# Kernel optimization log

Hardware: AMD Instinct MI355X
Metric: run time of the kernel (lower is better)

## Reference

```python
import jax, jax.numpy as jnp
import numpy as np

B, S, D, F, E, K = 2, 2048, 1024, 1024, 8, 2


def setup_inputs() -> dict:
    key = jax.random.key(0)
    kx, kg, k1, k3, k2 = jax.random.split(key, 5)
    # kaiming_uniform_(a=sqrt(5)) => Uniform(-1/sqrt(fan_in), 1/sqrt(fan_in))
    x = jax.random.normal(kx, (B, S, D), dtype=jnp.float32)
    gate_w = jax.random.uniform(kg, (E, D), jnp.float32, -1.0, 1.0) / np.sqrt(D)
    w1 = jax.random.uniform(k1, (E, F, D), jnp.float32, -1.0, 1.0) / np.sqrt(D)
    w3 = jax.random.uniform(k3, (E, F, D), jnp.float32, -1.0, 1.0) / np.sqrt(D)
    w2 = jax.random.uniform(k2, (E, D, F), jnp.float32, -1.0, 1.0) / np.sqrt(F)
    return {"x": x, "gate_w": gate_w, "w1": w1, "w3": w3, "w2": w2}


def reference(x, gate_w, w1, w3, w2):
    b, s, d = x.shape
    T = b * s
    xf = x.reshape(T, d)                      # [T, D]
    # ---- Gate: softmax scores, top-k selection, renormalized weights ----
    logits = xf @ gate_w.T                    # [T, E]
    probs = jax.nn.softmax(logits, axis=-1)
    topk_w, topk_idx = jax.lax.top_k(probs, K)            # [T, K]
    topk_w = topk_w / jnp.sum(topk_w, axis=-1, keepdims=True)
    # Dense per-token gate matrix [T, E]; zero for unselected experts, so the
    # weighted combine below is exactly sum_k w_k * expert_{idx_k}(x).
    gate_full = jnp.zeros((T, E), x.dtype).at[
        jnp.arange(T)[:, None], topk_idx].add(topk_w)
    # ---- Grouped SwiGLU experts: loop over small fixed E, vectorized over tokens ----
    out = jnp.zeros_like(xf)
    for e in range(E):
        h = jax.nn.silu(xf @ w1[e].T) * (xf @ w3[e].T)    # [T, F]
        out = out + gate_full[:, e:e + 1] * (h @ w2[e].T)  # [T, D]
    return out.reshape(b, s, d)
```

## Files before the change

kernel.cpp:

```cpp
#include <hip/hip_runtime.h>
#include <hip/hip_bf16.h>
#include <cstdint>
#include <cstddef>

#define T_TOK 4096
#define DDIM  1024
#define FDIM  1024
#define NEXP  8

typedef __attribute__((ext_vector_type(8))) short bf16x8;
typedef __attribute__((ext_vector_type(4))) float f32x4;
typedef __attribute__((ext_vector_type(8))) unsigned short u16x8;

__device__ __forceinline__ unsigned short f2bf(float f) {
  unsigned int u = __float_as_uint(f);
  u += 0x7FFFu + ((u >> 16) & 1u);
  return (unsigned short)(u >> 16);
}
__device__ __forceinline__ float bf2f(unsigned short u) {
  return __uint_as_float(((unsigned int)u) << 16);
}

__device__ __forceinline__ void gload_lds16(const void* g, void* l) {
  __builtin_amdgcn_global_load_lds(
      (const __attribute__((address_space(1))) unsigned int*)g,
      (__attribute__((address_space(3))) unsigned int*)l, 16, 0, 0);
}

__device__ __forceinline__ void vwait6() { asm volatile("s_waitcnt vmcnt(6)" ::: "memory"); }
__device__ __forceinline__ void vwait0() { asm volatile("s_waitcnt vmcnt(0)" ::: "memory"); }
__device__ __forceinline__ void lwait0() { asm volatile("s_waitcnt lgkmcnt(0)" ::: "memory"); }
__device__ __forceinline__ void barr()   { asm volatile("s_barrier" ::: "memory"); }

__device__ __forceinline__ bf16x8 frag_ld(const unsigned short* tile, int row, int kk) {
  int byteoff = (row << 7) + ((kk * 2) ^ ((row & 7) << 4));
  return *reinterpret_cast<const bf16x8*>(reinterpret_cast<const char*>(tile) + byteoff);
}

__global__ __launch_bounds__(256) void prep_kernel(
    const float* __restrict__ w1, const float* __restrict__ w3, const float* __restrict__ w2,
    unsigned short* __restrict__ W1b, unsigned short* __restrict__ W3b,
    unsigned short* __restrict__ W2b,
    const float* __restrict__ x, const float* __restrict__ gw,
    unsigned int* __restrict__ Xb32, int* __restrict__ tkidx, float* __restrict__ tkw,
    int* __restrict__ curp) {
  __shared__ float gws[NEXP * DDIM];
  const int bid = blockIdx.x;
  const int tid = threadIdx.x;

  if (bid < 3072) {
    const int sub = bid >> 10;
    const int b = bid & 1023;
    const float* s = (sub == 0) ? w1 : (sub == 1) ? w3 : w2;
    unsigned short* d = (sub == 0) ? W1b : (sub == 1) ? W3b : W2b;
    const int n = NEXP * FDIM * DDIM;
    const int stride = 1024 * 256 * 8;
    for (int i = (b * 256 + tid) * 8; i < n; i += stride) {
      float4 a = *reinterpret_cast<const float4*>(s + i);
      float4 c = *reinterpret_cast<const float4*>(s + i + 4);
      u16x8 o;
      o[0] = f2bf(a.x); o[1] = f2bf(a.y); o[2] = f2bf(a.z); o[3] = f2bf(a.w);
      o[4] = f2bf(c.x); o[5] = f2bf(c.y); o[6] = f2bf(c.z); o[7] = f2bf(c.w);
      *reinterpret_cast<u16x8*>(d + i) = o;
    }
    return;
  }

  const int lane = tid & 63;
  const int wid = tid >> 6;
  if (bid == 3072 && tid < NEXP) curp[tid * 32] = 0;
  for (int i = tid; i < NEXP * DDIM / 4; i += 256)
    reinterpret_cast<float4*>(gws)[i] = reinterpret_cast<const float4*>(gw)[i];
  __syncthreads();

  const int t = (bid - 3072) * 4 + wid;
  const float2* xr = reinterpret_cast<const float2*>(x + (size_t)t * DDIM);
  float2 xv[8];
#pragma unroll
  for (int i = 0; i < 8; ++i) xv[i] = xr[i * 64 + lane];
#pragma unroll
  for (int i = 0; i < 8; ++i)
    Xb32[(size_t)t * 512 + i * 64 + lane] =
        (unsigned int)f2bf(xv[i].x) | ((unsigned int)f2bf(xv[i].y) << 16);
  float p[NEXP];
#pragma unroll
  for (int e = 0; e < NEXP; ++e) p[e] = 0.f;
#pragma unroll
  for (int i = 0; i < 8; ++i) {
    const int k = (i * 64 + lane) * 2;
#pragma unroll
    for (int e = 0; e < NEXP; ++e)
      p[e] += xv[i].x * gws[e * DDIM + k] + xv[i].y * gws[e * DDIM + k + 1];
  }
#pragma unroll
  for (int s = 32; s > 0; s >>= 1)
#pragma unroll
    for (int e = 0; e < NEXP; ++e) p[e] += __shfl_xor(p[e], s, 64);
  if (lane == 0) {
    int i0 = 0; float l0 = p[0];
#pragma unroll
    for (int e = 1; e < NEXP; ++e) if (p[e] > l0) { l0 = p[e]; i0 = e; }
    int i1 = -1; float l1 = -1e30f;
#pragma unroll
    for (int e = 0; e < NEXP; ++e) if (e != i0 && p[e] > l1) { l1 = p[e]; i1 = e; }
    float ex = __expf(l1 - l0);
    float w0 = 1.f / (1.f + ex);
    float w1v = ex / (1.f + ex);
    tkidx[t * 2] = i0; tkidx[t * 2 + 1] = i1;
    tkw[t * 2] = w0;   tkw[t * 2 + 1] = w1v;
  }
}

__global__ __launch_bounds__(256) void fill_kernel(const int* __restrict__ tkidx,
                                                   const float* __restrict__ tkw,
                                                   int* __restrict__ offp,
                                                   int* __restrict__ curp,
                                                   int* __restrict__ list,
                                                   float* __restrict__ rgate) {
  __shared__ int ghist[4][NEXP];
  __shared__ int lhist[NEXP], base[NEXP];
  const int tid = threadIdx.x;
  if (tid < 32) ghist[tid >> 3][tid & 7] = 0;
  if (tid < NEXP) lhist[tid] = 0;
  __syncthreads();
  for (int i = tid; i < 2 * T_TOK; i += 256)
    atomicAdd(&ghist[tid >> 6][tkidx[i]], 1);
  const int t = blockIdx.x * 256 + tid;
  const int e0 = tkidx[t * 2], e1 = tkidx[t * 2 + 1];
  const int r0 = atomicAdd(&lhist[e0], 1);
  const int r1 = atomicAdd(&lhist[e1], 1);
  __syncthreads();
  if (tid < NEXP) {
    int o = 0;
#pragma unroll
    for (int j = 0; j < NEXP; ++j) {
      int c = ghist[0][j] + ghist[1][j] + ghist[2][j] + ghist[3][j];
      if (j < tid) o += c;
    }
    if (blockIdx.x == 0) {
      offp[tid] = o;
      if (tid == NEXP - 1)
        offp[NEXP] = o + ghist[0][tid] + ghist[1][tid] + ghist[2][tid] + ghist[3][tid];
    }
    base[tid] = o + atomicAdd(&curp[tid * 32], lhist[tid]);
  }
  __syncthreads();
  const int p0 = base[e0] + r0;
  const int p1 = base[e1] + r1;
  list[p0] = (t << 1);     rgate[p0] = tkw[t * 2];
  list[p1] = (t << 1) | 1; rgate[p1] = tkw[t * 2 + 1];
}

__global__ __launch_bounds__(256) void gemm1_kernel(
    const unsigned short* __restrict__ Xb, const unsigned short* __restrict__ W1b,
    const unsigned short* __restrict__ W3b, unsigned short* __restrict__ Hb,
    const int* __restrict__ off, const int* __restrict__ list) {
  const int e = blockIdx.y >> 5;
  const int rt = blockIdx.y & 31;
  const int seg0 = off[e];
  const int Ne = off[e + 1] - seg0;
  const int rowbase = rt * 128;
  if (rowbase >= Ne) return;
  const int f0 = blockIdx.x * 64;

  __shared__ unsigned short As[128 * 64];
  __shared__ unsigned short B1s[64 * 64];
  __shared__ unsigned short B3s[64 * 64];

  const int tid = threadIdx.x;
  const int lane = tid & 63;
  const int wid = tid >> 6;
  const int wr = wid >> 1, wc = wid & 1;

  int ldsoffA[4]; size_t abase[4];
  int ldsoffB[2]; size_t b1base[2];
#pragma unroll
  for (int j = 0; j < 4; ++j) {
    int boff = j * 4096 + wid * 1024 + lane * 16;
    int row = boff >> 7;
    int c = ((boff >> 4) & 7) ^ (row & 7);
    ldsoffA[j] = (j * 4096 + wid * 1024) >> 1;
    int ar = rowbase + row; if (ar > Ne - 1) ar = Ne - 1;
    int tok = list[seg0 + ar] >> 1;
    abase[j] = (size_t)tok * DDIM + c * 8;
  }
#pragma unroll
  for (int j = 0; j < 2; ++j) {
    int boff = j * 4096 + wid * 1024 + lane * 16;
    int row = boff >> 7;
    int c = ((boff >> 4) & 7) ^ (row & 7);
    ldsoffB[j] = (j * 4096 + wid * 1024) >> 1;
    b1base[j] = (size_t)(e * FDIM + f0 + row) * DDIM + c * 8;
  }

  f32x4 acc1[4][2], acc3[4][2];
  const f32x4 z = {0.f, 0.f, 0.f, 0.f};
#pragma unroll
  for (int m = 0; m < 4; ++m)
#pragma unroll
    for (int n = 0; n < 2; ++n) { acc1[m][n] = z; acc3[m][n] = z; }

  const int lrow = lane & 15;
  const int kb = (lane >> 4) * 8;
  for (int kt = 0; kt < DDIM / 64; ++kt) {
    const int ko = kt * 64;
#pragma unroll
    for (int j = 0; j < 4; ++j)
      gload_lds16(Xb + abase[j] + ko, &As[ldsoffA[j]]);
#pragma unroll
    for (int j = 0; j < 2; ++j) {
      gload_lds16(W1b + b1base[j] + ko, &B1s[ldsoffB[j]]);
      gload_lds16(W3b + b1base[j] + ko, &B3s[ldsoffB[j]]);
    }
    __syncthreads();
#pragma unroll
    for (int ks = 0; ks < 2; ++ks) {
      bf16x8 a[4], p[2], q[2];
#pragma unroll
      for (int m = 0; m < 4; ++m)
        a[m] = frag_ld(As, wr * 64 + m * 16 + lrow, ks * 32 + kb);
#pragma unroll
      for (int n = 0; n < 2; ++n) {
        p[n] = frag_ld(B1s, wc * 32 + n * 16 + lrow, ks * 32 + kb);
        q[n] = frag_ld(B3s, wc * 32 + n * 16 + lrow, ks * 32 + kb);
      }
#pragma unroll
      for (int m = 0; m < 4; ++m)
#pragma unroll
        for (int n = 0; n < 2; ++n) {
          acc1[m][n] = __builtin_amdgcn_mfma_f32_16x16x32_bf16(a[m], p[n], acc1[m][n], 0, 0, 0);
          acc3[m][n] = __builtin_amdgcn_mfma_f32_16x16x32_bf16(a[m], q[n], acc3[m][n], 0, 0, 0);
        }
    }
    __syncthreads();
  }

#pragma unroll
  for (int m = 0; m < 4; ++m)
#pragma unroll
    for (int n = 0; n < 2; ++n)
#pragma unroll
      for (int r = 0; r < 4; ++r) {
        int rloc = wr * 64 + m * 16 + ((lane >> 4) << 2) + r;
        if (rowbase + rloc < Ne) {
          float v1 = acc1[m][n][r], v3 = acc3[m][n][r];
          float h = v1 / (1.f + __expf(-v1)) * v3;
          int col = f0 + wc * 32 + n * 16 + (lane & 15);
          Hb[(size_t)(seg0 + rowbase + rloc) * FDIM + col] = f2bf(h);
        }
      }
}

__global__ __launch_bounds__(256) void gemm2_kernel(
    const unsigned short* __restrict__ Hb, const unsigned short* __restrict__ W2b,
    unsigned short* __restrict__ Yb, const int* __restrict__ off,
    const int* __restrict__ list, const float* __restrict__ rgate) {
  const int e = blockIdx.y >> 5;
  const int rt = blockIdx.y & 31;
  const int seg0 = off[e];
  const int Ne = off[e + 1] - seg0;
  const int rowbase = rt * 128;
  if (rowbase >= Ne) return;
  const int d0 = blockIdx.x * 64;

  __shared__ unsigned short As[2][128 * 64];
  __shared__ unsigned short Bs[2][64 * 64];

  const int tid = threadIdx.x;
  const int lane = tid & 63;
  const int wid = tid >> 6;
  const int wr = wid >> 1, wc = wid & 1;

  int ldsoffA[4]; size_t abase[4];
  int ldsoffB[2]; size_t bbase[2];
#pragma unroll
  for (int j = 0; j < 4; ++j) {
    int boff = j * 4096 + wid * 1024 + lane * 16;
    int row = boff >> 7;
    int c = ((boff >> 4) & 7) ^ (row & 7);
    ldsoffA[j] = (j * 4096 + wid * 1024) >> 1;
    int ar = rowbase + row; if (ar > Ne - 1) ar = Ne - 1;
    abase[j] = (size_t)(seg0 + ar) * FDIM + c * 8;
  }
#pragma unroll
  for (int j = 0; j < 2; ++j) {
    int boff = j * 4096 + wid * 1024 + lane * 16;
    int row = boff >> 7;
    int c = ((boff >> 4) & 7) ^ (row & 7);
    ldsoffB[j] = (j * 4096 + wid * 1024) >> 1;
    bbase[j] = (size_t)(e * DDIM + d0 + row) * FDIM + c * 8;
  }

  f32x4 acc[4][2];
  const f32x4 z = {0.f, 0.f, 0.f, 0.f};
#pragma unroll
  for (int m = 0; m < 4; ++m)
#pragma unroll
    for (int n = 0; n < 2; ++n) acc[m][n] = z;

  auto stage = [&](int buf, int kt) {
    const int ko = kt * 64;
#pragma unroll
    for (int j = 0; j < 4; ++j)
      gload_lds16(Hb + abase[j] + ko, &As[buf][ldsoffA[j]]);
#pragma unroll
    for (int j = 0; j < 2; ++j)
      gload_lds16(W2b + bbase[j] + ko, &Bs[buf][ldsoffB[j]]);
  };

  const int lrow = lane & 15;
  const int kb = (lane >> 4) * 8;

  vwait0();
  stage(0, 0);
  stage(1, 1);
  vwait6();
  barr();

  for (int t = 0; t < 16; ++t) {
    const int b = t & 1;
#pragma unroll
    for (int ks = 0; ks < 2; ++ks) {
      bf16x8 a[4], bb[2];
#pragma unroll
      for (int m = 0; m < 4; ++m)
        a[m] = frag_ld(As[b], wr * 64 + m * 16 + lrow, ks * 32 + kb);
#pragma unroll
      for (int n = 0; n < 2; ++n)
        bb[n] = frag_ld(Bs[b], wc * 32 + n * 16 + lrow, ks * 32 + kb);
#pragma unroll
      for (int m = 0; m < 4; ++m)
#pragma unroll
        for (int n = 0; n < 2; ++n)
          acc[m][n] = __builtin_amdgcn_mfma_f32_16x16x32_bf16(a[m], bb[n], acc[m][n], 0, 0, 0);
    }
    if (t == 15) break;
    lwait0();
    barr();
    if (t + 2 < 16) stage(b, t + 2);
    if (t < 14) vwait6(); else vwait0();
    barr();
  }

#pragma unroll
  for (int m = 0; m < 4; ++m)
#pragma unroll
    for (int r = 0; r < 4; ++r) {
      int rloc = wr * 64 + m * 16 + ((lane >> 4) << 2) + r;
      if (rowbase + rloc < Ne) {
        int rg = seg0 + rowbase + rloc;
        int tk = list[rg];
        float gsc = rgate[rg];
#pragma unroll
        for (int n = 0; n < 2; ++n) {
          int col = d0 + wc * 32 + n * 16 + (lane & 15);
          Yb[(size_t)tk * DDIM + col] = f2bf(gsc * acc[m][n][r]);
        }
      }
    }
}

__global__ __launch_bounds__(256) void combine_kernel(const unsigned short* __restrict__ Yb,
                                                      float* __restrict__ out) {
  const int n = T_TOK * DDIM / 8;
  const int stride = gridDim.x * blockDim.x;
  for (int i = blockIdx.x * blockDim.x + threadIdx.x; i < n; i += stride) {
    int t = i >> 7;
    int c = (i & 127) * 8;
    u16x8 a = *reinterpret_cast<const u16x8*>(Yb + ((size_t)t * 2) * DDIM + c);
    u16x8 b = *reinterpret_cast<const u16x8*>(Yb + ((size_t)t * 2 + 1) * DDIM + c);
    float4 o0, o1;
    o0.x = bf2f(a[0]) + bf2f(b[0]); o0.y = bf2f(a[1]) + bf2f(b[1]);
    o0.z = bf2f(a[2]) + bf2f(b[2]); o0.w = bf2f(a[3]) + bf2f(b[3]);
    o1.x = bf2f(a[4]) + bf2f(b[4]); o1.y = bf2f(a[5]) + bf2f(b[5]);
    o1.z = bf2f(a[6]) + bf2f(b[6]); o1.w = bf2f(a[7]) + bf2f(b[7]);
    float* dst = out + (size_t)t * DDIM + c;
    *reinterpret_cast<float4*>(dst) = o0;
    *reinterpret_cast<float4*>(dst + 4) = o1;
  }
}

extern "C" void kernel_launch(void* const* d_in, const int* in_sizes, int n_in,
                              void* d_out, int out_size, void* d_ws, size_t ws_size,
                              hipStream_t stream) {
  (void)in_sizes; (void)n_in; (void)ws_size; (void)out_size;
  const float* x  = (const float*)d_in[0];
  const float* gw = (const float*)d_in[1];
  const float* w1 = (const float*)d_in[2];
  const float* w3 = (const float*)d_in[3];
  const float* w2 = (const float*)d_in[4];
  float* out = (float*)d_out;

  char* ws = (char*)d_ws;
  unsigned short* Xb  = (unsigned short*)(ws + 0);
  unsigned short* W1b = (unsigned short*)(ws + 8388608);
  unsigned short* W3b = (unsigned short*)(ws + 25165824);
  unsigned short* W2b = (unsigned short*)(ws + 41943040);
  unsigned short* Hb  = (unsigned short*)(ws + 58720256);
  unsigned short* Yb  = (unsigned short*)(ws + 8388608);
  int*   ctrl  = (int*)(ws + 75497472);
  int*   off  = ctrl;
  int*   curp = ctrl + 16;
  int*   tkidx = (int*)(ws + 75497472 + 4096);
  float* tkw   = (float*)(ws + 75497472 + 4096 + 32768);
  int*   list  = (int*)(ws + 75497472 + 4096 + 65536);
  float* rgate = (float*)(ws + 75497472 + 4096 + 98304);

  prep_kernel<<<4096, 256, 0, stream>>>(w1, w3, w2, W1b, W3b, W2b,
                                        x, gw, (unsigned int*)Xb, tkidx, tkw, curp);
  fill_kernel<<<16, 256, 0, stream>>>(tkidx, tkw, off, curp, list, rgate);

  gemm1_kernel<<<dim3(16, 256), 256, 0, stream>>>(Xb, W1b, W3b, Hb, off, list);
  gemm2_kernel<<<dim3(16, 256), 256, 0, stream>>>(Hb, W2b, Yb, off, list, rgate);
  combine_kernel<<<2048, 256, 0, stream>>>(Yb, out);
}
```

Before: 135.4 us.

## Double-buffer gemm1 K-loop and overlap w2 bf16 conversion with gemm1

Moves the w2 fp32-to-bf16 conversion out of the prep kernel into 1024 extra leading blocks of the gemm1 launch, so the conversion can run alongside the expert GEMM blocks instead of before them. Gemm1's K-loop is rewritten to use 32-wide K tiles with two LDS buffers, prefetching tile t+2 while computing tile t, with explicit vmcnt waits and barriers and a matching swizzle for the 64-byte rows. This aims to hide global-load latency and shorten the serial prep phase. The cost is more barriers per K step, half-size tiles, and the conversion blocks competing with GEMM blocks for bandwidth and CUs.

After: 160.6 us. 1.19x slower.

```diff
diff --git a/kernel.cpp b/kernel.cpp
--- a/kernel.cpp
+++ b/kernel.cpp
@@ -28,6 +28,7 @@
 }
 
 __device__ __forceinline__ void vwait6() { asm volatile("s_waitcnt vmcnt(6)" ::: "memory"); }
+__device__ __forceinline__ void vwait4() { asm volatile("s_waitcnt vmcnt(4)" ::: "memory"); }
 __device__ __forceinline__ void vwait0() { asm volatile("s_waitcnt vmcnt(0)" ::: "memory"); }
 __device__ __forceinline__ void lwait0() { asm volatile("s_waitcnt lgkmcnt(0)" ::: "memory"); }
 __device__ __forceinline__ void barr()   { asm volatile("s_barrier" ::: "memory"); }
@@ -37,10 +38,14 @@
   return *reinterpret_cast<const bf16x8*>(reinterpret_cast<const char*>(tile) + byteoff);
 }
 
+__device__ __forceinline__ bf16x8 frag_ld32(const unsigned short* tile, int row, int kk) {
+  int byteoff = (row << 6) + ((kk * 2) ^ (((row >> 1) & 3) << 4));
+  return *reinterpret_cast<const bf16x8*>(reinterpret_cast<const char*>(tile) + byteoff);
+}
+
 __global__ __launch_bounds__(256) void prep_kernel(
-    const float* __restrict__ w1, const float* __restrict__ w3, const float* __restrict__ w2,
+    const float* __restrict__ w1, const float* __restrict__ w3,
     unsigned short* __restrict__ W1b, unsigned short* __restrict__ W3b,
-    unsigned short* __restrict__ W2b,
     const float* __restrict__ x, const float* __restrict__ gw,
     unsigned int* __restrict__ Xb32, int* __restrict__ tkidx, float* __restrict__ tkw,
     int* __restrict__ curp) {
@@ -48,11 +53,11 @@
   const int bid = blockIdx.x;
   const int tid = threadIdx.x;
 
-  if (bid < 3072) {
+  if (bid < 2048) {
     const int sub = bid >> 10;
     const int b = bid & 1023;
-    const float* s = (sub == 0) ? w1 : (sub == 1) ? w3 : w2;
-    unsigned short* d = (sub == 0) ? W1b : (sub == 1) ? W3b : W2b;
+    const float* s = (sub == 0) ? w1 : w3;
+    unsigned short* d = (sub == 0) ? W1b : W3b;
     const int n = NEXP * FDIM * DDIM;
     const int stride = 1024 * 256 * 8;
     for (int i = (b * 256 + tid) * 8; i < n; i += stride) {
@@ -68,12 +73,12 @@
 
   const int lane = tid & 63;
   const int wid = tid >> 6;
-  if (bid == 3072 && tid < NEXP) curp[tid * 32] = 0;
+  if (bid == 2048 && tid < NEXP) curp[tid * 32] = 0;
   for (int i = tid; i < NEXP * DDIM / 4; i += 256)
     reinterpret_cast<float4*>(gws)[i] = reinterpret_cast<const float4*>(gw)[i];
   __syncthreads();
 
-  const int t = (bid - 3072) * 4 + wid;
+  const int t = (bid - 2048) * 4 + wid;
   const float2* xr = reinterpret_cast<const float2*>(x + (size_t)t * DDIM);
   float2 xv[8];
 #pragma unroll
@@ -154,43 +159,62 @@
 __global__ __launch_bounds__(256) void gemm1_kernel(
     const unsigned short* __restrict__ Xb, const unsigned short* __restrict__ W1b,
     const unsigned short* __restrict__ W3b, unsigned short* __restrict__ Hb,
-    const int* __restrict__ off, const int* __restrict__ list) {
-  const int e = blockIdx.y >> 5;
-  const int rt = blockIdx.y & 31;
+    const int* __restrict__ off, const int* __restrict__ list,
+    const float* __restrict__ w2, unsigned short* __restrict__ W2b) {
+  const int bid0 = blockIdx.x;
+  const int tid = threadIdx.x;
+
+  if (bid0 < 1024) {
+    const int n = NEXP * FDIM * DDIM;
+    const int stride = 1024 * 256 * 8;
+    for (int i = (bid0 * 256 + tid) * 8; i < n; i += stride) {
+      float4 a = *reinterpret_cast<const float4*>(w2 + i);
+      float4 c = *reinterpret_cast<const float4*>(w2 + i + 4);
+      u16x8 o;
+      o[0] = f2bf(a.x); o[1] = f2bf(a.y); o[2] = f2bf(a.z); o[3] = f2bf(a.w);
+      o[4] = f2bf(c.x); o[5] = f2bf(c.y); o[6] = f2bf(c.z); o[7] = f2bf(c.w);
+      *reinterpret_cast<u16x8*>(W2b + i) = o;
+    }
+    return;
+  }
+
+  const int g = bid0 - 1024;
+  const int bx = g & 15;
+  const int by = g >> 4;
+  const int e = by >> 5;
+  const int rt = by & 31;
   const int seg0 = off[e];
   const int Ne = off[e + 1] - seg0;
   const int rowbase = rt * 128;
   if (rowbase >= Ne) return;
-  const int f0 = blockIdx.x * 64;
-
-  __shared__ unsigned short As[128 * 64];
-  __shared__ unsigned short B1s[64 * 64];
-  __shared__ unsigned short B3s[64 * 64];
-
-  const int tid = threadIdx.x;
+  const int f0 = bx * 64;
+
+  __shared__ unsigned short As[2][128 * 32];
+  __shared__ unsigned short B1s[2][64 * 32];
+  __shared__ unsigned short B3s[2][64 * 32];
+
   const int lane = tid & 63;
   const int wid = tid >> 6;
   const int wr = wid >> 1, wc = wid & 1;
 
-  int ldsoffA[4]; size_t abase[4];
-  int ldsoffB[2]; size_t b1base[2];
-#pragma unroll
-  for (int j = 0; j < 4; ++j) {
+  int ldsoffA[2]; size_t abase[2];
+#pragma unroll
+  for (int j = 0; j < 2; ++j) {
     int boff = j * 4096 + wid * 1024 + lane * 16;
-    int row = boff >> 7;
-    int c = ((boff >> 4) & 7) ^ (row & 7);
+    int row = boff >> 6;
+    int c = ((boff >> 4) & 3) ^ ((row >> 1) & 3);
     ldsoffA[j] = (j * 4096 + wid * 1024) >> 1;
     int ar = rowbase + row; if (ar > Ne - 1) ar = Ne - 1;
     int tok = list[seg0 + ar] >> 1;
     abase[j] = (size_t)tok * DDIM + c * 8;
   }
-#pragma unroll
-  for (int j = 0; j < 2; ++j) {
-    int boff = j * 4096 + wid * 1024 + lane * 16;
-    int row = boff >> 7;
-    int c = ((boff >> 4) & 7) ^ (row & 7);
-    ldsoffB[j] = (j * 4096 + wid * 1024) >> 1;
-    b1base[j] = (size_t)(e * FDIM + f0 + row) * DDIM + c * 8;
+  int ldsoffB; size_t bbase;
+  {
+    int boff = wid * 1024 + lane * 16;
+    int row = boff >> 6;
+    int c = ((boff >> 4) & 3) ^ ((row >> 1) & 3);
+    ldsoffB = (wid * 1024) >> 1;
+    bbase = (size_t)(e * FDIM + f0 + row) * DDIM + c * 8;
   }
 
   f32x4 acc1[4][2], acc3[4][2];
@@ -200,39 +224,48 @@
 #pragma unroll
     for (int n = 0; n < 2; ++n) { acc1[m][n] = z; acc3[m][n] = z; }
 
+  auto stage = [&](int buf, int kt) {
+    const int ko = kt * 32;
+#pragma unroll
+    for (int j = 0; j < 2; ++j)
+      gload_lds16(Xb + abase[j] + ko, &As[buf][ldsoffA[j]]);
+    gload_lds16(W1b + bbase + ko, &B1s[buf][ldsoffB]);
+    gload_lds16(W3b + bbase + ko, &B3s[buf][ldsoffB]);
+  };
+
   const int lrow = lane & 15;
   const int kb = (lane >> 4) * 8;
-  for (int kt = 0; kt < DDIM / 64; ++kt) {
-    const int ko = kt * 64;
-#pragma unroll
-    for (int j = 0; j < 4; ++j)
-      gload_lds16(Xb + abase[j] + ko, &As[ldsoffA[j]]);
-#pragma unroll
-    for (int j = 0; j < 2; ++j) {
-      gload_lds16(W1b + b1base[j] + ko, &B1s[ldsoffB[j]]);
-      gload_lds16(W3b + b1base[j] + ko, &B3s[ldsoffB[j]]);
-    }
-    __syncthreads();
-#pragma unroll
-    for (int ks = 0; ks < 2; ++ks) {
-      bf16x8 a[4], p[2], q[2];
-#pragma unroll
-      for (int m = 0; m < 4; ++m)
-        a[m] = frag_ld(As, wr * 64 + m * 16 + lrow, ks * 32 + kb);
+
+  vwait0();
+  stage(0, 0);
+  stage(1, 1);
+  vwait4();
+  barr();
+
+  for (int t = 0; t < 32; ++t) {
+    const int b = t & 1;
+    bf16x8 a[4], p[2], q[2];
+#pragma unroll
+    for (int m = 0; m < 4; ++m)
+      a[m] = frag_ld32(&As[b][0], wr * 64 + m * 16 + lrow, kb);
+#pragma unroll
+    for (int n = 0; n < 2; ++n) {
+      p[n] = frag_ld32(&B1s[b][0], wc * 32 + n * 16 + lrow, kb);
+      q[n] = frag_ld32(&B3s[b][0], wc * 32 + n * 16 + lrow, kb);
+    }
+#pragma unroll
+    for (int m = 0; m < 4; ++m)
 #pragma unroll
       for (int n = 0; n < 2; ++n) {
-        p[n] = frag_ld(B1s, wc * 32 + n * 16 + lrow, ks * 32 + kb);
-        q[n] = frag_ld(B3s, wc * 32 + n * 16 + lrow, ks * 32 + kb);
+        acc1[m][n] = __builtin_amdgcn_mfma_f32_16x16x32_bf16(a[m], p[n], acc1[m][n], 0, 0, 0);
+        acc3[m][n] = __builtin_amdgcn_mfma_f32_16x16x32_bf16(a[m], q[n], acc3[m][n], 0, 0, 0);
       }
-#pragma unroll
-      for (int m = 0; m < 4; ++m)
-#pragma unroll
-        for (int n = 0; n < 2; ++n) {
-          acc1[m][n] = __builtin_amdgcn_mfma_f32_16x16x32_bf16(a[m], p[n], acc1[m][n], 0, 0, 0);
-          acc3[m][n] = __builtin_amdgcn_mfma_f32_16x16x32_bf16(a[m], q[n], acc3[m][n], 0, 0, 0);
-        }
-    }
-    __syncthreads();
+    if (t == 31) break;
+    lwait0();
+    barr();
+    if (t + 2 < 32) stage(b, t + 2);
+    if (t < 30) vwait4(); else vwait0();
+    barr();
   }
 
 #pragma unroll
@@ -406,11 +439,11 @@
   int*   list  = (int*)(ws + 75497472 + 4096 + 65536);
   float* rgate = (float*)(ws + 75497472 + 4096 + 98304);
 
-  prep_kernel<<<4096, 256, 0, stream>>>(w1, w3, w2, W1b, W3b, W2b,
+  prep_kernel<<<3072, 256, 0, stream>>>(w1, w3, W1b, W3b,
                                         x, gw, (unsigned int*)Xb, tkidx, tkw, curp);
   fill_kernel<<<16, 256, 0, stream>>>(tkidx, tkw, off, curp, list, rgate);
 
-  gemm1_kernel<<<dim3(16, 256), 256, 0, stream>>>(Xb, W1b, W3b, Hb, off, list);
+  gemm1_kernel<<<1024 + 4096, 256, 0, stream>>>(Xb, W1b, W3b, Hb, off, list, w2, W2b);
   gemm2_kernel<<<dim3(16, 256), 256, 0, stream>>>(Hb, W2b, Yb, off, list, rgate);
   combine_kernel<<<2048, 256, 0, stream>>>(Yb, out);
 }
```

## Move w2 bf16 conversion into gemm1 launch to overlap with expert GEMM

Applied to the files above, without the earlier changes.

Takes the fp32-to-bf16 conversion of w2 out of the prep kernel and gives it to 1024 extra blocks appended to the gemm1 launch. The grid is flattened to 1D, and block indices at or above 4096 perform the conversion. The intent is to overlap this memory-bound conversion with the compute-bound first expert GEMM instead of serializing it before routing. Because the extra blocks sit at the end of the grid, they may run only after most GEMM blocks are scheduled, which would limit the overlap.

Measured after the change: 131.9 us. -2.6%, faster.

```diff
diff --git a/kernel.cpp b/kernel.cpp
--- a/kernel.cpp
+++ b/kernel.cpp
@@ -38,9 +38,8 @@
 }
 
 __global__ __launch_bounds__(256) void prep_kernel(
-    const float* __restrict__ w1, const float* __restrict__ w3, const float* __restrict__ w2,
+    const float* __restrict__ w1, const float* __restrict__ w3,
     unsigned short* __restrict__ W1b, unsigned short* __restrict__ W3b,
-    unsigned short* __restrict__ W2b,
     const float* __restrict__ x, const float* __restrict__ gw,
     unsigned int* __restrict__ Xb32, int* __restrict__ tkidx, float* __restrict__ tkw,
     int* __restrict__ curp) {
@@ -48,11 +47,11 @@
   const int bid = blockIdx.x;
   const int tid = threadIdx.x;
 
-  if (bid < 3072) {
+  if (bid < 2048) {
     const int sub = bid >> 10;
     const int b = bid & 1023;
-    const float* s = (sub == 0) ? w1 : (sub == 1) ? w3 : w2;
-    unsigned short* d = (sub == 0) ? W1b : (sub == 1) ? W3b : W2b;
+    const float* s = (sub == 0) ? w1 : w3;
+    unsigned short* d = (sub == 0) ? W1b : W3b;
     const int n = NEXP * FDIM * DDIM;
     const int stride = 1024 * 256 * 8;
     for (int i = (b * 256 + tid) * 8; i < n; i += stride) {
@@ -68,12 +67,12 @@
 
   const int lane = tid & 63;
   const int wid = tid >> 6;
-  if (bid == 3072 && tid < NEXP) curp[tid * 32] = 0;
+  if (bid == 2048 && tid < NEXP) curp[tid * 32] = 0;
   for (int i = tid; i < NEXP * DDIM / 4; i += 256)
     reinterpret_cast<float4*>(gws)[i] = reinterpret_cast<const float4*>(gw)[i];
   __syncthreads();
 
-  const int t = (bid - 3072) * 4 + wid;
+  const int t = (bid - 2048) * 4 + wid;
   const float2* xr = reinterpret_cast<const float2*>(x + (size_t)t * DDIM);
   float2 xv[8];
 #pragma unroll
@@ -154,20 +153,40 @@
 __global__ __launch_bounds__(256) void gemm1_kernel(
     const unsigned short* __restrict__ Xb, const unsigned short* __restrict__ W1b,
     const unsigned short* __restrict__ W3b, unsigned short* __restrict__ Hb,
-    const int* __restrict__ off, const int* __restrict__ list) {
-  const int e = blockIdx.y >> 5;
-  const int rt = blockIdx.y & 31;
+    const int* __restrict__ off, const int* __restrict__ list,
+    const float* __restrict__ w2, unsigned short* __restrict__ W2b) {
+  const int bid0 = blockIdx.x;
+  const int tid = threadIdx.x;
+
+  if (bid0 >= 4096) {
+    const int b = bid0 - 4096;
+    const int n = NEXP * FDIM * DDIM;
+    const int stride = 1024 * 256 * 8;
+    for (int i = (b * 256 + tid) * 8; i < n; i += stride) {
+      float4 a = *reinterpret_cast<const float4*>(w2 + i);
+      float4 c = *reinterpret_cast<const float4*>(w2 + i + 4);
+      u16x8 o;
+      o[0] = f2bf(a.x); o[1] = f2bf(a.y); o[2] = f2bf(a.z); o[3] = f2bf(a.w);
+      o[4] = f2bf(c.x); o[5] = f2bf(c.y); o[6] = f2bf(c.z); o[7] = f2bf(c.w);
+      *reinterpret_cast<u16x8*>(W2b + i) = o;
+    }
+    return;
+  }
+
+  const int bx = bid0 & 15;
+  const int by = bid0 >> 4;
+  const int e = by >> 5;
+  const int rt = by & 31;
   const int seg0 = off[e];
   const int Ne = off[e + 1] - seg0;
   const int rowbase = rt * 128;
   if (rowbase >= Ne) return;
-  const int f0 = blockIdx.x * 64;
+  const int f0 = bx * 64;
 
   __shared__ unsigned short As[128 * 64];
   __shared__ unsigned short B1s[64 * 64];
   __shared__ unsigned short B3s[64 * 64];
 
-  const int tid = threadIdx.x;
   const int lane = tid & 63;
   const int wid = tid >> 6;
   const int wr = wid >> 1, wc = wid & 1;
@@ -406,11 +425,11 @@
   int*   list  = (int*)(ws + 75497472 + 4096 + 65536);
   float* rgate = (float*)(ws + 75497472 + 4096 + 98304);
 
-  prep_kernel<<<4096, 256, 0, stream>>>(w1, w3, w2, W1b, W3b, W2b,
+  prep_kernel<<<3072, 256, 0, stream>>>(w1, w3, W1b, W3b,
                                         x, gw, (unsigned int*)Xb, tkidx, tkw, curp);
   fill_kernel<<<16, 256, 0, stream>>>(tkidx, tkw, off, curp, list, rgate);
 
-  gemm1_kernel<<<dim3(16, 256), 256, 0, stream>>>(Xb, W1b, W3b, Hb, off, list);
+  gemm1_kernel<<<4096 + 1024, 256, 0, stream>>>(Xb, W1b, W3b, Hb, off, list, w2, W2b);
   gemm2_kernel<<<dim3(16, 256), 256, 0, stream>>>(Hb, W2b, Yb, off, list, rgate);
   combine_kernel<<<2048, 256, 0, stream>>>(Yb, out);
 }
```
